# Performance work log

Hardware: AMD Instinct MI355X
Metric: run time of the kernel (lower is better)

## Reference

```python
import jax, jax.numpy as jnp
import numpy as np

H = 32  # rnn/encoder/residual hidden dim
NEG = -1e9


def gru(x, h0, Wih, Whh, bih, bhh):
    # x: (B,T,D), h0: (B,H); torch GRU gate order [r,z,n]
    xp = jnp.swapaxes(x @ Wih.T + bih, 0, 1)  # (T,B,3H)

    def step(h, xt):
        gh = h @ Whh.T + bhh
        xr, xz, xn = jnp.split(xt, 3, axis=-1)
        hr, hz, hn = jnp.split(gh, 3, axis=-1)
        r = jax.nn.sigmoid(xr + hr)
        z = jax.nn.sigmoid(xz + hz)
        n = jnp.tanh(xn + r * hn)
        h_new = (1.0 - z) * n + z * h
        return h_new, h_new

    hT, ys = jax.lax.scan(step, h0, xp)
    return jnp.swapaxes(ys, 0, 1), hT  # (B,T,H), (B,H)


def setup_inputs():
    key = jax.random.key(0)
    ks = jax.random.split(key, 30)
    B, T = 2048, 128
    def lin(k, o, i):
        return jax.random.normal(k, (o, i), jnp.float32) / np.sqrt(i)
    inp = {}
    inp['obs'] = jax.random.normal(ks[0], (B, T, 15), jnp.float32)
    inp['rnn_state'] = jax.random.normal(ks[1], (1, B, 3 * H), jnp.float32)
    inp['enc_air_W'] = lin(ks[2], H, 7); inp['enc_air_b'] = jnp.zeros((H,), jnp.float32)
    inp['enc_m_W'] = lin(ks[3], H, 4); inp['enc_m_b'] = jnp.zeros((H,), jnp.float32)
    inp['air_Wih'] = lin(ks[4], 3 * H, H); inp['air_Whh'] = lin(ks[5], 3 * H, H)
    inp['air_bih'] = jnp.zeros((3 * H,), jnp.float32); inp['air_bhh'] = jnp.zeros((3 * H,), jnp.float32)
    inp['m_Wih'] = lin(ks[6], 3 * H, H); inp['m_Whh'] = lin(ks[7], 3 * H, H)
    inp['m_bih'] = jnp.zeros((3 * H,), jnp.float32); inp['m_bhh'] = jnp.zeros((3 * H,), jnp.float32)
    inp['attn_in_w'] = lin(ks[8], 3 * H, H); inp['attn_in_b'] = jnp.zeros((3 * H,), jnp.float32)
    inp['attn_out_w'] = lin(ks[9], H, H); inp['attn_out_b'] = jnp.zeros((H,), jnp.float32)
    inp['mlp_W0'] = lin(ks[10], 256, 2 * H); inp['mlp_b0'] = jnp.zeros((256,), jnp.float32)
    inp['mlp_W1'] = lin(ks[11], 256, 256); inp['mlp_b1'] = jnp.zeros((256,), jnp.float32)
    inp['out_W'] = lin(ks[12], 1, 256); inp['out_b'] = jnp.zeros((1,), jnp.float32)
    return inp


def reference(obs, rnn_state, enc_air_W, enc_air_b, enc_m_W, enc_m_b,
              air_Wih, air_Whh, air_bih, air_bhh,
              m_Wih, m_Whh, m_bih, m_bhh,
              attn_in_w, attn_in_b, attn_out_w, attn_out_b,
              mlp_W0, mlp_b0, mlp_W1, mlp_b1, out_W, out_b):
    B, T, _ = obs.shape
    h_air0 = rnn_state[0, :, :H]                       # (B,H)
    h_m0 = rnn_state[0, :, H:].reshape(2 * B, H)       # faithful reshape (1,B,64)->(1,2B,32)

    # aircraft branch
    air_emb = obs[..., 8:] @ enc_air_W.T + enc_air_b   # (B,T,H)
    air_feat, next_h_air = gru(air_emb, h_air0, air_Wih, air_Whh, air_bih, air_bhh)

    # missile branch: concat missiles along batch dim
    m_raw = jnp.concatenate([obs[..., 0:4], obs[..., 4:8]], axis=0)  # (2B,T,4)
    m_emb = m_raw @ enc_m_W.T + enc_m_b
    m_feat, next_h_m = gru(m_emb, h_m0, m_Wih, m_Whh, m_bih, m_bhh)
    m1_feat, m2_feat = m_feat[:B], m_feat[B:]

    # inactive-missile mask from raw obs
    obs_flat = obs.reshape(-1, 15)
    inact = jnp.array([1.0, 0.0, 1.0, 0.0], jnp.float32)
    mask = jnp.stack([
        jnp.all(jnp.isclose(obs_flat[:, 0:4], inact), axis=-1),
        jnp.all(jnp.isclose(obs_flat[:, 4:8], inact), axis=-1),
    ], axis=1)                                          # (N,2) True = masked

    N = B * T
    air_flat = air_feat.reshape(N, H)
    m1_flat = m1_feat.reshape(N, H)
    m2_flat = m2_feat.reshape(N, H)

    # 2-head attention, q len 1, kv len 2
    Wq, Wk, Wv = jnp.split(attn_in_w, 3, axis=0)
    bq, bk, bv = jnp.split(attn_in_b, 3, axis=0)
    nh, hd = 2, H // 2
    qh = (air_flat @ Wq.T + bq).reshape(N, nh, hd)
    kv = jnp.stack([m1_flat, m2_flat], axis=1)          # (N,2,H)
    kh = (kv @ Wk.T + bk).reshape(N, 2, nh, hd)
    vh = (kv @ Wv.T + bv).reshape(N, 2, nh, hd)
    scores = jnp.einsum('nhd,nkhd->nhk', qh, kh) / np.sqrt(hd)
    scores = scores + jnp.where(mask[:, None, :], NEG, 0.0)
    w = jax.nn.softmax(scores, axis=-1)
    ctx = jnp.einsum('nhk,nkhd->nhd', w, vh).reshape(N, H)
    attn = ctx @ attn_out_w.T + attn_out_b
    attn = jnp.where(jnp.all(mask, axis=-1, keepdims=True), 0.0, attn)  # torch nan_to_num(all-masked)

    fusion = jnp.concatenate([air_flat, attn], axis=-1)  # (N,2H)
    h1 = jax.nn.leaky_relu(fusion @ mlp_W0.T + mlp_b0, 0.01)
    h2 = jax.nn.leaky_relu(h1 @ mlp_W1.T + mlp_b1, 0.01)
    val = h2 @ out_W.T + out_b                           # (N,1)

    next_h = jnp.concatenate([next_h_air, next_h_m.reshape(B, 2 * H)], axis=-1)[None]  # (1,B,96)
    return val, next_h
```

## Files before the change

kernel.cpp:

```cpp
#include <hip/hip_runtime.h>
#include <hip/hip_bf16.h>

#define BB 2048
#define TT 128
#define NN (BB*TT)
#define NVAL NN

#define OFF_W0P   2048u
#define OFF_W1P   10240u
#define OFF_WQKV  43008u
#define OFF_WO    44544u
#define OFF_PWHA  49792u
#define OFF_PWHM  51328u
#define OFF_PWCA  52864u
#define OFF_PWCM  54400u
#define OFF_BHNA  55936u
#define OFF_BHNM  55968u
#define OFF_AIRF  83968u
#define OFF_MF    4278272u
#define OFF_MASK  12666880u

#define L2E 1.44269504088896341f

typedef __attribute__((ext_vector_type(8))) short short8;
typedef __attribute__((ext_vector_type(4))) float f32x4;
typedef _Float16 f16x8 __attribute__((ext_vector_type(8)));
typedef unsigned u32x4 __attribute__((ext_vector_type(4)));

__device__ __forceinline__ unsigned short f2bf(float f) {
    unsigned u = __builtin_bit_cast(unsigned, f);
    u += 0x7FFFu + ((u >> 16) & 1u);
    return (unsigned short)(u >> 16);
}
__device__ __forceinline__ unsigned f2h(float f) {
    _Float16 h = (_Float16)f;
    return (unsigned)__builtin_bit_cast(unsigned short, h);
}
__device__ __forceinline__ unsigned pkh2(float a, float b) {
    return (f2h(b) << 16) | f2h(a);
}
__device__ __forceinline__ float fast_rcp(float x) {
    return __builtin_amdgcn_rcpf(x);
}
__device__ __forceinline__ float ex2(float x) {
    return __builtin_amdgcn_exp2f(x);
}
__device__ __forceinline__ unsigned cvt_pk_bf16(float a, float b) {
    unsigned r;
    asm("v_cvt_pk_bf16_f32 %0, %1, %2" : "=v"(r) : "v"(a), "v"(b));
    return r;
}
__device__ __forceinline__ f32x4 mfma16f(f16x8 a, f16x8 b, f32x4 c) {
    return __builtin_amdgcn_mfma_f32_16x16x32_f16(a, b, c, 0, 0, 0);
}
__device__ __forceinline__ f32x4 mfma16b(short8 a, short8 b, f32x4 c) {
    return __builtin_amdgcn_mfma_f32_16x16x32_bf16(a, b, c, 0, 0, 0);
}
__device__ __forceinline__ float lrelu(float h) {
    return (h > 0.f) ? h : 0.01f*h;
}

__global__ __launch_bounds__(256) void prep_kernel(
    const float* __restrict__ enc_air_W, const float* __restrict__ enc_air_b,
    const float* __restrict__ enc_m_W,   const float* __restrict__ enc_m_b,
    const float* __restrict__ air_Wih,   const float* __restrict__ air_bih,
    const float* __restrict__ m_Wih,     const float* __restrict__ m_bih,
    const float* __restrict__ air_Whh,   const float* __restrict__ m_Whh,
    const float* __restrict__ air_bhh,   const float* __restrict__ m_bhh,
    const float* __restrict__ W0,        const float* __restrict__ W1,
    const float* __restrict__ attn_in_w, const float* __restrict__ attn_out_w,
    float* __restrict__ ws)
{
    int b = blockIdx.x, t = threadIdx.x;
    if (b == 0) {
    } else if (b <= 32) {
        unsigned short* w1p = (unsigned short*)(ws + OFF_W1P);
        int base = ((b-1)*256 + t);
        int lane = base & 63;
        int ctf  = base >> 6;
        int ft2  = ctf & 15, kap = ctf >> 4;
        int col = lane & 15, quad = lane >> 4;
        int o  = ft2*16 + col;
        #pragma unroll
        for (int j = 0; j < 8; j++) {
            int f = (2*kap + (j>>2))*16 + quad*4 + (j&3);
            w1p[base*8 + j] = f2bf(W1[o*256 + f]);
        }
    } else if (b <= 40) {
        unsigned short* w0p = (unsigned short*)(ws + OFF_W0P);
        int base = ((b-33)*256 + t);
        int lane = base & 63;
        int ctf  = base >> 6;
        int ct   = ctf & 15, s = ctf >> 4;
        int col = lane & 15, quad = lane >> 4;
        int k0 = s*32 + quad*8;
        int o  = ct*16 + col;
        #pragma unroll
        for (int j = 0; j < 8; j++)
            w0p[base*8 + j] = f2bf(W0[o*64 + k0 + j]);
    } else if (b == 41) {
        unsigned short* wqkv = (unsigned short*)(ws + OFF_WQKV);
        unsigned short* wop  = (unsigned short*)(ws + OFF_WO);
        for (int slot = t; slot < 512; slot += 256) {
            if (slot < 384) {
                int ct = slot >> 6, lane = slot & 63;
                int col = lane & 15, quad = lane >> 4;
                int o = ct*16 + col;
                #pragma unroll
                for (int j = 0; j < 8; j++)
                    wqkv[slot*8 + j] = f2bf(attn_in_w[o*32 + quad*8 + j]);
            } else {
                int s2 = slot - 384;
                int ct = s2 >> 6, lane = s2 & 63;
                int col = lane & 15, quad = lane >> 4;
                #pragma unroll
                for (int j = 0; j < 8; j++)
                    wop[s2*8 + j] = f2bf(attn_out_w[(ct*16+col)*32 + quad*8 + j]);
            }
        }
    } else if (b == 42) {
        unsigned* pa = (unsigned*)(ws + OFF_PWHA);
        unsigned* pm = (unsigned*)(ws + OFF_PWHM);
        for (int s = t; s < 3072; s += 256) {
            int s2 = (s < 1536) ? s : s - 1536;
            const float* W = (s < 1536) ? air_Whh : m_Whh;
            unsigned* dst = (s < 1536) ? pa : pm;
            int tile = s2 >> 8;
            int l    = (s2 >> 2) & 63;
            int d    = s2 & 3;
            int gate = tile >> 1, hfp = tile & 1;
            int rr = l & 15;
            int f  = (rr >> 2)*8 + hfp*4 + (rr & 3);
            int k  = (l >> 4)*8 + d*2;
            int row = gate*32 + f;
            float sc = (gate == 2) ? 2.f*L2E : L2E;
            dst[s2] = pkh2(W[row*32 + k]*sc, W[row*32 + k + 1]*sc);
        }
    } else {
        unsigned* pa = (unsigned*)(ws + OFF_PWCA);
        unsigned* pm = (unsigned*)(ws + OFF_PWCM);
        for (int s = t; s < 3072; s += 256) {
            bool isA = (s < 1536);
            int s2 = isA ? s : s - 1536;
            unsigned* dst = isA ? pa : pm;
            int tile = s2 >> 8, l = (s2 >> 2) & 63, d = s2 & 3;
            int gate = tile >> 1, hfp = tile & 1;
            int rr = l & 15;
            int f = (rr >> 2)*8 + hfp*4 + (rr & 3);
            int o = gate*32 + f;
            int kb = (l >> 4)*8 + d*2;
            int ni = isA ? 7 : 4;
            float sc = (gate == 2) ? 2.f*L2E : L2E;
            float v[2];
            #pragma unroll
            for (int e = 0; e < 2; e++) {
                int k = kb + e;
                float acc = 0.f;
                if (k < ni) {
                    for (int m = 0; m < 32; m++)
                        acc += isA ? air_Wih[o*32+m]*enc_air_W[m*7+k]
                                   : m_Wih[o*32+m]*enc_m_W[m*4+k];
                } else if (k == ni) {
                    acc = isA ? air_bih[o] : m_bih[o];
                    for (int m = 0; m < 32; m++)
                        acc += isA ? air_Wih[o*32+m]*enc_air_b[m]
                                   : m_Wih[o*32+m]*enc_m_b[m];
                    if (gate < 2) acc += isA ? air_bhh[o] : m_bhh[o];
                }
                v[e] = acc*sc;
            }
            dst[s2] = pkh2(v[0], v[1]);
        }
        if (t < 32) {
            ws[OFF_BHNA + t] = air_bhh[64 + t]*2.f*L2E;
            ws[OFF_BHNM + t] = m_bhh[64 + t]*2.f*L2E;
        }
    }
}

template<bool AIRT>
__device__ __forceinline__ void gru_tile(
    const float* __restrict__ obs, const float* __restrict__ rnn,
    const float* __restrict__ ws,
    unsigned short* __restrict__ feat, float* __restrict__ mask_f,
    float* __restrict__ nh_out, int tileIdx, unsigned* __restrict__ XH)
{
    const int lane = threadIdx.x & 63;
    const int col = lane & 15, quad = lane >> 4;

    const unsigned* pw = (const unsigned*)(ws + (AIRT ? OFF_PWHA : OFF_PWHM));
    const unsigned* pc = (const unsigned*)(ws + (AIRT ? OFF_PWCA : OFF_PWCM));
    f16x8 whf[6], wcf[6];
    #pragma unroll
    for (int i6 = 0; i6 < 6; i6++) {
        whf[i6] = __builtin_bit_cast(f16x8, *(const u32x4*)(pw + i6*256 + lane*4));
        wcf[i6] = __builtin_bit_cast(f16x8, *(const u32x4*)(pc + i6*256 + lane*4));
    }
    const float* bhnp = ws + (AIRT ? OFF_BHNA : OFF_BHNM) + quad*8;
    f32x4 bhn0 = *(const f32x4*)(bhnp);
    f32x4 bhn1 = *(const f32x4*)(bhnp + 4);

    int slot = 0, tb;
    if (AIRT) { tb = tileIdx*16; }
    else      { slot = tileIdx >> 7; tb = (tileIdx & 127)*16; }

    {
        const int coff = AIRT ? 8 : slot*4;
        #pragma unroll 4
        for (int it = 0; it < 32; it++) {
            int s = it*64 + lane;
            int r = s >> 7, t = s & 127;
            const float* p = obs + (size_t)(tb + r)*1920 + t*15 + coff;
            unsigned d0, d1, d2, d3;
            if (AIRT) {
                d0 = pkh2(p[0], p[1]); d1 = pkh2(p[2], p[3]);
                d2 = pkh2(p[4], p[5]); d3 = pkh2(p[6], 1.0f);
            } else {
                float x0 = p[0], x1 = p[1], x2 = p[2], x3 = p[3];
                d0 = pkh2(x0, x1); d1 = pkh2(x2, x3);
                d2 = 0x00003C00u; d3 = 0u;
                bool ok = (fabsf(x0 - 1.f) <= 1.00001e-5f) && (fabsf(x1) <= 1e-8f) &&
                          (fabsf(x2 - 1.f) <= 1.00001e-5f) && (fabsf(x3) <= 1e-8f);
                mask_f[((size_t)(tb + r)*TT + t)*2 + slot] = ok ? 1.f : 0.f;
            }
            unsigned off = (unsigned)(r*512 + 4*(t ^ (r & 7)));
            *(u32x4*)(XH + off) = (u32x4){d0, d1, d2, d3};
        }
    }
    __syncthreads();

    int rowi = tileIdx*16 + col;
    int hbase;
    if (AIRT) hbase = rowi*96;
    else      hbase = (rowi >> 1)*96 + 32 + (rowi & 1)*32;
    unsigned short* featp = feat + (size_t)rowi*(TT*32) + quad*8;

    f32x4 h0v = *(const f32x4*)(rnn + hbase + quad*8);
    f32x4 h1v = *(const f32x4*)(rnn + hbase + quad*8 + 4);

    const int xk = col & 7;
    const unsigned bidx = (unsigned)col*512;
    const f32x4 z4 = {0.f, 0.f, 0.f, 0.f};

    f32x4 gx0, gx1, gx2, gx3, gx4, gx5;
    {
        u32x4 xc = *(const u32x4*)(XH + bidx + 4u*(unsigned)(0 ^ xk));
        f16x8 xf = __builtin_bit_cast(f16x8, xc);
        gx0 = mfma16f(wcf[0], xf, z4); gx1 = mfma16f(wcf[1], xf, z4);
        gx2 = mfma16f(wcf[2], xf, z4); gx3 = mfma16f(wcf[3], xf, z4);
        gx4 = mfma16f(wcf[4], xf, z4); gx5 = mfma16f(wcf[5], xf, z4);
    }
    u32x4 xA = *(const u32x4*)(XH + bidx + 4u*(unsigned)(1 ^ xk));
    u32x4 xB = *(const u32x4*)(XH + bidx + 4u*(unsigned)(2 ^ xk));

    #pragma unroll 1
    for (int t = 0; t < TT; t += 2) {
        f32x4 gy0, gy1, gy2, gy3, gy4, gy5;
        {
            u32x4 hdv;
            hdv[0] = pkh2(h0v[0], h0v[1]); hdv[1] = pkh2(h0v[2], h0v[3]);
            hdv[2] = pkh2(h1v[0], h1v[1]); hdv[3] = pkh2(h1v[2], h1v[3]);
            f16x8 hff = __builtin_bit_cast(f16x8, hdv);

            f32x4 aR0 = mfma16f(whf[0], hff, gx0);
            f32x4 aR1 = mfma16f(whf[1], hff, gx1);
            f32x4 aZ0 = mfma16f(whf[2], hff, gx2);
            f32x4 aZ1 = mfma16f(whf[3], hff, gx3);
            f32x4 aHN0 = mfma16f(whf[4], hff, bhn0);
            f32x4 aHN1 = mfma16f(whf[5], hff, bhn1);
            f32x4 aXN0 = gx4, aXN1 = gx5;

            f16x8 xf1 = __builtin_bit_cast(f16x8, xA);
            gy0 = mfma16f(wcf[0], xf1, z4); gy1 = mfma16f(wcf[1], xf1, z4);
            gy2 = mfma16f(wcf[2], xf1, z4); gy3 = mfma16f(wcf[3], xf1, z4);
            gy4 = mfma16f(wcf[4], xf1, z4); gy5 = mfma16f(wcf[5], xf1, z4);
            const int tp = (t+3 < TT) ? t+3 : TT-1;
            xA = *(const u32x4*)(XH + bidx + 4u*(unsigned)(tp ^ xk));

            #pragma unroll
            for (int s = 0; s < 4; s++) {
                {
                    float r = fast_rcp(1.f + ex2(-aR0[s]));
                    float z = fast_rcp(1.f + ex2(-aZ0[s]));
                    float p = aXN0[s] + r*aHN0[s];
                    float n = fmaf(-2.f, fast_rcp(1.f + ex2(p)), 1.f);
                    h0v[s] = n + z*(h0v[s] - n);
                }
                {
                    float r = fast_rcp(1.f + ex2(-aR1[s]));
                    float z = fast_rcp(1.f + ex2(-aZ1[s]));
                    float p = aXN1[s] + r*aHN1[s];
                    float n = fmaf(-2.f, fast_rcp(1.f + ex2(p)), 1.f);
                    h1v[s] = n + z*(h1v[s] - n);
                }
            }

            u32x4 fwE;
            fwE[0] = cvt_pk_bf16(h0v[0], h0v[1]); fwE[1] = cvt_pk_bf16(h0v[2], h0v[3]);
            fwE[2] = cvt_pk_bf16(h1v[0], h1v[1]); fwE[3] = cvt_pk_bf16(h1v[2], h1v[3]);
            *(u32x4*)(featp + (size_t)t*32) = fwE;
        }
        {
            u32x4 hdv2;
            hdv2[0] = pkh2(h0v[0], h0v[1]); hdv2[1] = pkh2(h0v[2], h0v[3]);
            hdv2[2] = pkh2(h1v[0], h1v[1]); hdv2[3] = pkh2(h1v[2], h1v[3]);
            f16x8 hff2 = __builtin_bit_cast(f16x8, hdv2);

            f32x4 bR0 = mfma16f(whf[0], hff2, gy0);
            f32x4 bR1 = mfma16f(whf[1], hff2, gy1);
            f32x4 bZ0 = mfma16f(whf[2], hff2, gy2);
            f32x4 bZ1 = mfma16f(whf[3], hff2, gy3);
            f32x4 bHN0 = mfma16f(whf[4], hff2, bhn0);
            f32x4 bHN1 = mfma16f(whf[5], hff2, bhn1);
            f32x4 bXN0 = gy4, bXN1 = gy5;

            f16x8 xf2 = __builtin_bit_cast(f16x8, xB);
            gx0 = mfma16f(wcf[0], xf2, z4); gx1 = mfma16f(wcf[1], xf2, z4);
            gx2 = mfma16f(wcf[2], xf2, z4); gx3 = mfma16f(wcf[3], xf2, z4);
            gx4 = mfma16f(wcf[4], xf2, z4); gx5 = mfma16f(wcf[5], xf2, z4);
            const int tq = (t+4 < TT) ? t+4 : TT-1;
            xB = *(const u32x4*)(XH + bidx + 4u*(unsigned)(tq ^ xk));

            #pragma unroll
            for (int s = 0; s < 4; s++) {
                {
                    float r = fast_rcp(1.f + ex2(-bR0[s]));
                    float z = fast_rcp(1.f + ex2(-bZ0[s]));
                    float p = bXN0[s] + r*bHN0[s];
                    float n = fmaf(-2.f, fast_rcp(1.f + ex2(p)), 1.f);
                    h0v[s] = n + z*(h0v[s] - n);
                }
                {
                    float r = fast_rcp(1.f + ex2(-bR1[s]));
                    float z = fast_rcp(1.f + ex2(-bZ1[s]));
                    float p = bXN1[s] + r*bHN1[s];
                    float n = fmaf(-2.f, fast_rcp(1.f + ex2(p)), 1.f);
                    h1v[s] = n + z*(h1v[s] - n);
                }
            }

            u32x4 fwO;
            fwO[0] = cvt_pk_bf16(h0v[0], h0v[1]); fwO[1] = cvt_pk_bf16(h0v[2], h0v[3]);
            fwO[2] = cvt_pk_bf16(h1v[0], h1v[1]); fwO[3] = cvt_pk_bf16(h1v[2], h1v[3]);
            *(u32x4*)(featp + (size_t)(t+1)*32) = fwO;
        }
    }
    *(f32x4*)(nh_out + hbase + quad*8)     = h0v;
    *(f32x4*)(nh_out + hbase + quad*8 + 4) = h1v;
}

__global__ __launch_bounds__(64, 1) void gru_kernel(
    const float* __restrict__ obs, const float* __restrict__ rnn,
    const float* __restrict__ ws,
    unsigned short* __restrict__ air_feat, unsigned short* __restrict__ m_feat,
    float* __restrict__ mask_f, float* __restrict__ nh_out)
{
    __shared__ unsigned XH[8192];
    int g = blockIdx.x;
    if (g < 128) gru_tile<true >(obs, rnn, ws, air_feat, mask_f, nh_out, g, XH);
    else         gru_tile<false>(obs, rnn, ws, m_feat,  mask_f, nh_out, g - 128, XH);
}

__global__ __launch_bounds__(512, 4) void fused_kernel(
    const unsigned short* __restrict__ air_feat, const unsigned short* __restrict__ m_feat,
    const float* __restrict__ mask_f,
    const unsigned short* __restrict__ wqkv, const float* __restrict__ attn_in_b,
    const unsigned short* __restrict__ wop,  const float* __restrict__ attn_out_b,
    const unsigned short* __restrict__ w0p, const float* __restrict__ b0,
    const unsigned short* __restrict__ w1p, const float* __restrict__ b1,
    const float* __restrict__ outW, const float* __restrict__ outb,
    float* __restrict__ val)
{
    __shared__ unsigned short XB[16384];
    __shared__ unsigned short AT[4096];
    __shared__ float PS[8][64];

    unsigned short* CT = XB;

    const int tid  = threadIdx.x;
    const int lane = tid & 63;
    const int wid  = tid >> 6;
    const int col  = lane & 15;
    const int quad = lane >> 4;
    const size_t n0 = (size_t)blockIdx.x * 64;
    const int rt    = wid & 3;
    const int tbase = (wid >> 2) * 8;

    short8 w0f0[8];
    #pragma unroll
    for (int i = 0; i < 8; i++)
        w0f0[i] = *(const short8*)(w0p + ((tbase + i)*64 + lane)*8);
    short8 bAir = *(const short8*)(air_feat + (n0 + rt*16 + col)*32 + quad*8);

    f32x4 accL1[8];
    #pragma unroll
    for (int i = 0; i < 8; i++) accL1[i] = (f32x4){0.f,0.f,0.f,0.f};

    if (wid < 4) {
        const int strip = wid;
        short8 wqf[2], wkf[2], wvf[2], wof[2];
        #pragma unroll
        for (int ct = 0; ct < 2; ct++) {
            wqf[ct] = *(const short8*)(wqkv + ((0+ct)*64 + lane)*8);
            wkf[ct] = *(const short8*)(wqkv + ((2+ct)*64 + lane)*8);
            wvf[ct] = *(const short8*)(wqkv + ((4+ct)*64 + lane)*8);
            wof[ct] = *(const short8*)(wop + (ct*64 + lane)*8);
        }
        short8 a_m1 = *(const short8*)(m_feat + (n0 + strip*16 + col)*32 + quad*8);
        short8 a_m2 = *(const short8*)(m_feat + ((size_t)NN + n0 + strip*16 + col)*32 + quad*8);

        float m0a[4], m1a[4];
        #pragma unroll
        for (int reg = 0; reg < 4; reg++) {
            const float* mp = mask_f + (size_t)(n0 + strip*16 + quad*4 + reg)*2;
            m0a[reg] = mp[0]; m1a[reg] = mp[1];
        }

        f32x4 q[2], k1[2], k2[2], v1[2], v2[2], ao[2];
        #pragma unroll
        for (int ct = 0; ct < 2; ct++) {
            f32x4 z = (f32x4){0.f,0.f,0.f,0.f};
            q[ct]  = mfma16b(bAir, wqf[ct], z);
            k1[ct] = mfma16b(a_m1, wkf[ct], z);
            k2[ct] = mfma16b(a_m2, wkf[ct], z);
            v1[ct] = mfma16b(a_m1, wvf[ct], z);
            v2[ct] = mfma16b(a_m2, wvf[ct], z);
        }
        float bqr[2], bkr[2], bvr[2];
        #pragma unroll
        for (int ct = 0; ct < 2; ct++) {
            bqr[ct] = attn_in_b[ct*16 + col];
            bkr[ct] = attn_in_b[32 + ct*16 + col];
            bvr[ct] = attn_in_b[64 + ct*16 + col];
        }
        float p1s[2][4], p2s[2][4];
        #pragma unroll
        for (int ct = 0; ct < 2; ct++) {
            #pragma unroll
            for (int reg = 0; reg < 4; reg++) {
                float qq = q[ct][reg] + bqr[ct];
                float p1 = qq * (k1[ct][reg] + bkr[ct]);
                float p2 = qq * (k2[ct][reg] + bkr[ct]);
                #pragma unroll
                for (int m = 1; m < 16; m <<= 1) {
                    p1 += __shfl_xor(p1, m, 64);
                    p2 += __shfl_xor(p2, m, 64);
                }
                p1s[ct][reg] = p1; p2s[ct][reg] = p2;
            }
        }
        float bothm[4];
        #pragma unroll
        for (int reg = 0; reg < 4; reg++) {
            int rloc = strip*16 + quad*4 + reg;
            float m0v = m0a[reg], m1v = m1a[reg];
            bothm[reg] = (m0v > 0.5f && m1v > 0.5f) ? 1.f : 0.f;
            #pragma unroll
            for (int ct = 0; ct < 2; ct++) {
                float s1 = p1s[ct][reg]*0.25f + (m0v > 0.5f ? -1e9f : 0.f);
                float s2 = p2s[ct][reg]*0.25f + (m1v > 0.5f ? -1e9f : 0.f);
                float mx = fmaxf(s1, s2);
                float e1 = __expf(s1 - mx), e2 = __expf(s2 - mx);
                float inv = fast_rcp(e1 + e2);
                float ctxv = ((v1[ct][reg] + bvr[ct])*e1 +
                              (v2[ct][reg] + bvr[ct])*e2) * inv;
                CT[rloc*40 + ct*16 + col] = f2bf(ctxv);
            }
        }
        short8 a_ctx = *(const short8*)&CT[(strip*16 + col)*40 + quad*8];
        #pragma unroll
        for (int ct = 0; ct < 2; ct++) {
            f32x4 z = (f32x4){0.f,0.f,0.f,0.f};
            ao[ct] = mfma16b(a_ctx, wof[ct], z);
        }
        float bor[2] = { attn_out_b[col], attn_out_b[16 + col] };
        #pragma unroll
        for (int reg = 0; reg < 4; reg++) {
            #pragma unroll
            for (int ct = 0; ct < 2; ct++) {
                float av = ao[ct][reg] + bor[ct];
                av = (bothm[reg] > 0.5f) ? 0.f : av;
                AT[strip*1024 + (quad*4 + reg)*64 + ct*16 + col] = f2bf(av);
            }
        }
    } else {
        #pragma unroll
        for (int i = 0; i < 8; i++)
            accL1[i] = mfma16b(w0f0[i], bAir, accL1[i]);
    }
    __syncthreads();

    if (wid < 4) {
        #pragma unroll
        for (int i = 0; i < 8; i++)
            accL1[i] = mfma16b(w0f0[i], bAir, accL1[i]);
    }
    {
        short8 bAttn = *(const short8*)&AT[rt*1024 + col*64 + quad*8];
        #pragma unroll
        for (int i = 0; i < 8; i++) {
            short8 w0f1 = *(const short8*)(w0p + ((16 + tbase + i)*64 + lane)*8);
            accL1[i] = mfma16b(w0f1, bAttn, accL1[i]);
        }
    }
    #pragma unroll
    for (int i = 0; i < 8; i += 2) {
        int t0 = tbase + i;
        f32x4 bA = *(const f32x4*)(b0 + t0*16 + quad*4);
        f32x4 bB = *(const f32x4*)(b0 + (t0+1)*16 + quad*4);
        float a0 = lrelu(accL1[i][0]   + bA[0]), a1 = lrelu(accL1[i][1]   + bA[1]);
        float a2 = lrelu(accL1[i][2]   + bA[2]), a3 = lrelu(accL1[i][3]   + bA[3]);
        float c0 = lrelu(accL1[i+1][0] + bB[0]), c1 = lrelu(accL1[i+1][1] + bB[1]);
        float c2 = lrelu(accL1[i+1][2] + bB[2]), c3 = lrelu(accL1[i+1][3] + bB[3]);
        u32x4 w;
        w[0] = cvt_pk_bf16(a0, a1); w[1] = cvt_pk_bf16(a2, a3);
        w[2] = cvt_pk_bf16(c0, c1); w[3] = cvt_pk_bf16(c2, c3);
        int kap = t0 >> 1;
        *(u32x4*)((unsigned*)XB + ((rt*8 + kap)*64 + lane)*4) = w;
    }
    __syncthreads();

    f32x4 acc2[4][2];
    #pragma unroll
    for (int r = 0; r < 4; r++)
        #pragma unroll
        for (int c = 0; c < 2; c++) acc2[r][c] = (f32x4){0.f,0.f,0.f,0.f};
    {
        short8 w1f[2], w1n[2];
        #pragma unroll
        for (int c = 0; c < 2; c++)
            w1f[c] = *(const short8*)(w1p + ((0*16 + wid*2 + c)*64 + lane)*8);
        #pragma unroll
        for (int kap = 0; kap < 8; kap++) {
            if (kap < 7) {
                #pragma unroll
                for (int c = 0; c < 2; c++)
                    w1n[c] = *(const short8*)(w1p + (((kap+1)*16 + wid*2 + c)*64 + lane)*8);
            }
            short8 bx[4];
            #pragma unroll
            for (int r = 0; r < 4; r++)
                bx[r] = *(const short8*)&XB[((r*8 + kap)*64 + lane)*8];
            #pragma unroll
            for (int c = 0; c < 2; c++)
                #pragma unroll
                for (int r = 0; r < 4; r++)
                    acc2[r][c] = mfma16b(w1f[c], bx[r], acc2[r][c]);
            #pragma unroll
            for (int c = 0; c < 2; c++) w1f[c] = w1n[c];
        }
    }

    f32x4 b1v[2], owv[2];
    #pragma unroll
    for (int c = 0; c < 2; c++) {
        b1v[c] = *(const f32x4*)(b1 + (wid*2 + c)*16 + quad*4);
        owv[c] = *(const f32x4*)(outW + (wid*2 + c)*16 + quad*4);
    }
    const float outb0 = outb[0];
    #pragma unroll
    for (int r = 0; r < 4; r++) {
        float pv = 0.f;
        #pragma unroll
        for (int c = 0; c < 2; c++) {
            #pragma unroll
            for (int reg = 0; reg < 4; reg++) {
                float h = lrelu(acc2[r][c][reg] + b1v[c][reg]);
                pv += h*owv[c][reg];
            }
        }
        pv += __shfl_xor(pv, 16, 64);
        pv += __shfl_xor(pv, 32, 64);
        if (lane < 16) PS[wid][r*16 + lane] = pv;
    }
    __syncthreads();
    if (tid < 64)
        val[n0 + tid] = PS[0][tid] + PS[1][tid] + PS[2][tid] + PS[3][tid]
                      + PS[4][tid] + PS[5][tid] + PS[6][tid] + PS[7][tid] + outb0;
}

extern "C" void kernel_launch(void* const* d_in, const int* in_sizes, int n_in,
                              void* d_out, int out_size, void* d_ws, size_t ws_size,
                              hipStream_t stream) {
    const float* obs        = (const float*)d_in[0];
    const float* rnn        = (const float*)d_in[1];
    const float* enc_air_W  = (const float*)d_in[2];
    const float* enc_air_b  = (const float*)d_in[3];
    const float* enc_m_W    = (const float*)d_in[4];
    const float* enc_m_b    = (const float*)d_in[5];
    const float* air_Wih    = (const float*)d_in[6];
    const float* air_Whh    = (const float*)d_in[7];
    const float* air_bih    = (const float*)d_in[8];
    const float* air_bhh    = (const float*)d_in[9];
    const float* m_Wih      = (const float*)d_in[10];
    const float* m_Whh      = (const float*)d_in[11];
    const float* m_bih      = (const float*)d_in[12];
    const float* m_bhh      = (const float*)d_in[13];
    const float* attn_in_w  = (const float*)d_in[14];
    const float* attn_in_b  = (const float*)d_in[15];
    const float* attn_out_w = (const float*)d_in[16];
    const float* attn_out_b = (const float*)d_in[17];
    const float* mlp_W0     = (const float*)d_in[18];
    const float* mlp_b0     = (const float*)d_in[19];
    const float* mlp_W1     = (const float*)d_in[20];
    const float* mlp_b1     = (const float*)d_in[21];
    const float* out_W      = (const float*)d_in[22];
    const float* out_b      = (const float*)d_in[23];

    float* ws  = (float*)d_ws;
    float* out = (float*)d_out;

    prep_kernel<<<44, 256, 0, stream>>>(enc_air_W, enc_air_b, enc_m_W, enc_m_b,
                                        air_Wih, air_bih, m_Wih, m_bih,
                                        air_Whh, m_Whh, air_bhh, m_bhh,
                                        mlp_W0, mlp_W1, attn_in_w, attn_out_w, ws);

    gru_kernel<<<384, 64, 0, stream>>>(obs, rnn, ws,
                                       (unsigned short*)(ws + OFF_AIRF),
                                       (unsigned short*)(ws + OFF_MF),
                                       ws + OFF_MASK, out + NVAL);

    fused_kernel<<<NN/64, 512, 0, stream>>>((const unsigned short*)(ws + OFF_AIRF),
                                            (const unsigned short*)(ws + OFF_MF),
                                            ws + OFF_MASK,
                                            (const unsigned short*)(ws + OFF_WQKV), attn_in_b,
                                            (const unsigned short*)(ws + OFF_WO),   attn_out_b,
                                            (const unsigned short*)(ws + OFF_W0P), mlp_b0,
                                            (const unsigned short*)(ws + OFF_W1P), mlp_b1,
                                            out_W, out_b, out);
}
```

Measured before the change: 300.6 us.

## Spread attention across all eight waves and alias LDS buffers for higher occupancy

The attention Q/K/V and softmax stage now runs on all eight waves, each handling one strip and one head, instead of only four waves doing both heads. The attention-output and partial-sum buffers share one LDS array, and the launch bound is raised from 4 to 6 blocks per CU. This is meant to cut the serial attention phase in which half the waves sat idle, and to allow more resident blocks. The cost is an extra block barrier, mask values read twice, and tighter register limits that may cause spills.

```diff
diff --git a/kernel.cpp b/kernel.cpp
--- a/kernel.cpp
+++ b/kernel.cpp
@@ -361,7 +361,7 @@
     else         gru_tile<false>(obs, rnn, ws, m_feat,  mask_f, nh_out, g - 128, XH);
 }
 
-__global__ __launch_bounds__(512, 4) void fused_kernel(
+__global__ __launch_bounds__(512, 6) void fused_kernel(
     const unsigned short* __restrict__ air_feat, const unsigned short* __restrict__ m_feat,
     const float* __restrict__ mask_f,
     const unsigned short* __restrict__ wqkv, const float* __restrict__ attn_in_b,
@@ -372,10 +372,11 @@
     float* __restrict__ val)
 {
     __shared__ unsigned short XB[16384];
-    __shared__ unsigned short AT[4096];
-    __shared__ float PS[8][64];
+    __shared__ unsigned short ATPS[4096];
 
     unsigned short* CT = XB;
+    unsigned short* AT = ATPS;
+    float* PS = (float*)ATPS;
 
     const int tid  = threadIdx.x;
     const int lane = tid & 63;
@@ -383,117 +384,89 @@
     const int col  = lane & 15;
     const int quad = lane >> 4;
     const size_t n0 = (size_t)blockIdx.x * 64;
+    const int strip = wid >> 1;
+    const int act   = wid & 1;
     const int rt    = wid & 3;
     const int tbase = (wid >> 2) * 8;
 
+    const f32x4 z4 = {0.f, 0.f, 0.f, 0.f};
+
+    {
+        short8 wq = *(const short8*)(wqkv + ((0+act)*64 + lane)*8);
+        short8 wk = *(const short8*)(wqkv + ((2+act)*64 + lane)*8);
+        short8 wv = *(const short8*)(wqkv + ((4+act)*64 + lane)*8);
+        short8 bAirA = *(const short8*)(air_feat + (n0 + strip*16 + col)*32 + quad*8);
+        short8 a_m1 = *(const short8*)(m_feat + (n0 + strip*16 + col)*32 + quad*8);
+        short8 a_m2 = *(const short8*)(m_feat + ((size_t)NN + n0 + strip*16 + col)*32 + quad*8);
+
+        f32x4 q  = mfma16b(bAirA, wq, z4);
+        f32x4 k1 = mfma16b(a_m1, wk, z4);
+        f32x4 k2 = mfma16b(a_m2, wk, z4);
+        f32x4 v1 = mfma16b(a_m1, wv, z4);
+        f32x4 v2 = mfma16b(a_m2, wv, z4);
+        float bq = attn_in_b[act*16 + col];
+        float bk = attn_in_b[32 + act*16 + col];
+        float bv = attn_in_b[64 + act*16 + col];
+
+        #pragma unroll
+        for (int reg = 0; reg < 4; reg++) {
+            float qq = q[reg] + bq;
+            float p1 = qq * (k1[reg] + bk);
+            float p2 = qq * (k2[reg] + bk);
+            #pragma unroll
+            for (int m = 1; m < 16; m <<= 1) {
+                p1 += __shfl_xor(p1, m, 64);
+                p2 += __shfl_xor(p2, m, 64);
+            }
+            const float* mp = mask_f + (size_t)(n0 + strip*16 + quad*4 + reg)*2;
+            float m0v = mp[0], m1v = mp[1];
+            float s1 = p1*0.25f + (m0v > 0.5f ? -1e9f : 0.f);
+            float s2 = p2*0.25f + (m1v > 0.5f ? -1e9f : 0.f);
+            float mx = fmaxf(s1, s2);
+            float e1 = __expf(s1 - mx), e2 = __expf(s2 - mx);
+            float inv = fast_rcp(e1 + e2);
+            float ctxv = ((v1[reg] + bv)*e1 + (v2[reg] + bv)*e2) * inv;
+            CT[(strip*16 + quad*4 + reg)*40 + act*16 + col] = f2bf(ctxv);
+        }
+    }
+    __syncthreads();
+
+    f32x4 accL1[8];
+    #pragma unroll
+    for (int i = 0; i < 8; i++) accL1[i] = z4;
     short8 w0f0[8];
     #pragma unroll
     for (int i = 0; i < 8; i++)
         w0f0[i] = *(const short8*)(w0p + ((tbase + i)*64 + lane)*8);
-    short8 bAir = *(const short8*)(air_feat + (n0 + rt*16 + col)*32 + quad*8);
-
-    f32x4 accL1[8];
-    #pragma unroll
-    for (int i = 0; i < 8; i++) accL1[i] = (f32x4){0.f,0.f,0.f,0.f};
+    short8 bAirL = *(const short8*)(air_feat + (n0 + rt*16 + col)*32 + quad*8);
 
     if (wid < 4) {
-        const int strip = wid;
-        short8 wqf[2], wkf[2], wvf[2], wof[2];
-        #pragma unroll
-        for (int ct = 0; ct < 2; ct++) {
-            wqf[ct] = *(const short8*)(wqkv + ((0+ct)*64 + lane)*8);
-            wkf[ct] = *(const short8*)(wqkv + ((2+ct)*64 + lane)*8);
-            wvf[ct] = *(const short8*)(wqkv + ((4+ct)*64 + lane)*8);
-            wof[ct] = *(const short8*)(wop + (ct*64 + lane)*8);
-        }
-        short8 a_m1 = *(const short8*)(m_feat + (n0 + strip*16 + col)*32 + quad*8);
-        short8 a_m2 = *(const short8*)(m_feat + ((size_t)NN + n0 + strip*16 + col)*32 + quad*8);
-
-        float m0a[4], m1a[4];
+        short8 wof0 = *(const short8*)(wop + (0*64 + lane)*8);
+        short8 wof1 = *(const short8*)(wop + (1*64 + lane)*8);
+        short8 a_ctx = *(const short8*)&CT[(wid*16 + col)*40 + quad*8];
+        f32x4 ao0 = mfma16b(a_ctx, wof0, z4);
+        f32x4 ao1 = mfma16b(a_ctx, wof1, z4);
+        float bor0 = attn_out_b[col], bor1 = attn_out_b[16 + col];
         #pragma unroll
         for (int reg = 0; reg < 4; reg++) {
-            const float* mp = mask_f + (size_t)(n0 + strip*16 + quad*4 + reg)*2;
-            m0a[reg] = mp[0]; m1a[reg] = mp[1];
-        }
-
-        f32x4 q[2], k1[2], k2[2], v1[2], v2[2], ao[2];
-        #pragma unroll
-        for (int ct = 0; ct < 2; ct++) {
-            f32x4 z = (f32x4){0.f,0.f,0.f,0.f};
-            q[ct]  = mfma16b(bAir, wqf[ct], z);
-            k1[ct] = mfma16b(a_m1, wkf[ct], z);
-            k2[ct] = mfma16b(a_m2, wkf[ct], z);
-            v1[ct] = mfma16b(a_m1, wvf[ct], z);
-            v2[ct] = mfma16b(a_m2, wvf[ct], z);
-        }
-        float bqr[2], bkr[2], bvr[2];
-        #pragma unroll
-        for (int ct = 0; ct < 2; ct++) {
-            bqr[ct] = attn_in_b[ct*16 + col];
-            bkr[ct] = attn_in_b[32 + ct*16 + col];
-            bvr[ct] = attn_in_b[64 + ct*16 + col];
-        }
-        float p1s[2][4], p2s[2][4];
-        #pragma unroll
-        for (int ct = 0; ct < 2; ct++) {
-            #pragma unroll
-            for (int reg = 0; reg < 4; reg++) {
-                float qq = q[ct][reg] + bqr[ct];
-                float p1 = qq * (k1[ct][reg] + bkr[ct]);
-                float p2 = qq * (k2[ct][reg] + bkr[ct]);
-                #pragma unroll
-                for (int m = 1; m < 16; m <<= 1) {
-                    p1 += __shfl_xor(p1, m, 64);
-                    p2 += __shfl_xor(p2, m, 64);
-                }
-                p1s[ct][reg] = p1; p2s[ct][reg] = p2;
-            }
-        }
-        float bothm[4];
-        #pragma unroll
-        for (int reg = 0; reg < 4; reg++) {
-            int rloc = strip*16 + quad*4 + reg;
-            float m0v = m0a[reg], m1v = m1a[reg];
-            bothm[reg] = (m0v > 0.5f && m1v > 0.5f) ? 1.f : 0.f;
-            #pragma unroll
-            for (int ct = 0; ct < 2; ct++) {
-                float s1 = p1s[ct][reg]*0.25f + (m0v > 0.5f ? -1e9f : 0.f);
-                float s2 = p2s[ct][reg]*0.25f + (m1v > 0.5f ? -1e9f : 0.f);
-                float mx = fmaxf(s1, s2);
-                float e1 = __expf(s1 - mx), e2 = __expf(s2 - mx);
-                float inv = fast_rcp(e1 + e2);
-                float ctxv = ((v1[ct][reg] + bvr[ct])*e1 +
-                              (v2[ct][reg] + bvr[ct])*e2) * inv;
-                CT[rloc*40 + ct*16 + col] = f2bf(ctxv);
-            }
-        }
-        short8 a_ctx = *(const short8*)&CT[(strip*16 + col)*40 + quad*8];
-        #pragma unroll
-        for (int ct = 0; ct < 2; ct++) {
-            f32x4 z = (f32x4){0.f,0.f,0.f,0.f};
-            ao[ct] = mfma16b(a_ctx, wof[ct], z);
-        }
-        float bor[2] = { attn_out_b[col], attn_out_b[16 + col] };
-        #pragma unroll
-        for (int reg = 0; reg < 4; reg++) {
-            #pragma unroll
-            for (int ct = 0; ct < 2; ct++) {
-                float av = ao[ct][reg] + bor[ct];
-                av = (bothm[reg] > 0.5f) ? 0.f : av;
-                AT[strip*1024 + (quad*4 + reg)*64 + ct*16 + col] = f2bf(av);
-            }
+            const float* mp = mask_f + (size_t)(n0 + wid*16 + quad*4 + reg)*2;
+            bool both = (mp[0] > 0.5f) && (mp[1] > 0.5f);
+            float av0 = both ? 0.f : (ao0[reg] + bor0);
+            float av1 = both ? 0.f : (ao1[reg] + bor1);
+            AT[wid*1024 + (quad*4 + reg)*64 + col] = f2bf(av0);
+            AT[wid*1024 + (quad*4 + reg)*64 + 16 + col] = f2bf(av1);
         }
     } else {
         #pragma unroll
         for (int i = 0; i < 8; i++)
-            accL1[i] = mfma16b(w0f0[i], bAir, accL1[i]);
+            accL1[i] = mfma16b(w0f0[i], bAirL, accL1[i]);
     }
     __syncthreads();
 
     if (wid < 4) {
         #pragma unroll
         for (int i = 0; i < 8; i++)
-            accL1[i] = mfma16b(w0f0[i], bAir, accL1[i]);
+            accL1[i] = mfma16b(w0f0[i], bAirL, accL1[i]);
     }
     {
         short8 bAttn = *(const short8*)&AT[rt*1024 + col*64 + quad*8];
@@ -524,7 +497,7 @@
     #pragma unroll
     for (int r = 0; r < 4; r++)
         #pragma unroll
-        for (int c = 0; c < 2; c++) acc2[r][c] = (f32x4){0.f,0.f,0.f,0.f};
+        for (int c = 0; c < 2; c++) acc2[r][c] = z4;
     {
         short8 w1f[2], w1n[2];
         #pragma unroll
@@ -571,12 +544,12 @@
         }
         pv += __shfl_xor(pv, 16, 64);
         pv += __shfl_xor(pv, 32, 64);
-        if (lane < 16) PS[wid][r*16 + lane] = pv;
+        if (lane < 16) PS[wid*64 + r*16 + lane] = pv;
     }
     __syncthreads();
     if (tid < 64)
-        val[n0 + tid] = PS[0][tid] + PS[1][tid] + PS[2][tid] + PS[3][tid]
-                      + PS[4][tid] + PS[5][tid] + PS[6][tid] + PS[7][tid] + outb0;
+        val[n0 + tid] = PS[0*64 + tid] + PS[1*64 + tid] + PS[2*64 + tid] + PS[3*64 + tid]
+                      + PS[4*64 + tid] + PS[5*64 + tid] + PS[6*64 + tid] + PS[7*64 + tid] + outb0;
 }
 
 extern "C" void kernel_launch(void* const* d_in, const int* in_sizes, int n_in,
```

After: 298.4 us. No clear change (-0.7%).
